# Optimization experiments

Hardware: AMD Instinct MI355X
Metric: run time of the kernel (lower is better)

Reference implementation:

```python
import jax, jax.numpy as jnp
import numpy as np

HEADS = 16
HEAD_SIZE = 64
INF = 1e12  # bert4keras K.infinity() uses a large finite value


def _rotate_interleaved(x):
    # result[..., 2i] = -x[..., 2i+1]; result[..., 2i+1] = x[..., 2i]
    x2 = jnp.stack([-x[..., 1::2], x[..., ::2]], axis=-1)
    return x2.reshape(x.shape)


def setup_inputs() -> dict:
    key = jax.random.key(0)
    k1, k2 = jax.random.split(key)
    B, N, D = 8, 1024, 1024
    x = jax.random.normal(k1, (B, N, D), dtype=jnp.float32)
    W = jax.random.normal(k2, (D, 2 * HEADS * HEAD_SIZE), dtype=jnp.float32) * (1.0 / np.sqrt(D))
    b = jnp.zeros((2 * HEADS * HEAD_SIZE,), dtype=jnp.float32)
    seq_mask = jnp.ones((B, N), dtype=jnp.float32)
    return {"x": x, "W": W, "b": b, "seq_mask": seq_mask}


def reference(x, W, b, seq_mask):
    B, N, _ = x.shape
    H, d = HEADS, HEAD_SIZE
    proj = x @ W + b                       # [B, N, 2*H*d]
    z = proj.reshape(B, N, H, 2 * d)       # split into heads then stack
    qw, kw = z[..., :d], z[..., d:]        # [B, N, H, d]

    # RoPE (interleaved sin/cos)
    pos = jnp.arange(N, dtype=jnp.float32)
    freqs = jnp.power(10000.0, -2.0 * jnp.arange(d // 2, dtype=jnp.float32) / d)
    ang = pos[:, None] * freqs[None, :]    # [N, d/2]
    cos_pos = jnp.repeat(jnp.cos(ang), 2, axis=-1)[None, :, None, :]  # [1,N,1,d]
    sin_pos = jnp.repeat(jnp.sin(ang), 2, axis=-1)[None, :, None, :]
    qw = qw * cos_pos + _rotate_interleaved(qw) * sin_pos
    kw = kw * cos_pos + _rotate_interleaved(kw) * sin_pos

    logits = jnp.einsum('bmhd,bnhd->bhmn', qw, kw)   # [B, H, N, N]

    # sequence masking on query (axis 2) and key (axis 3)
    logits = logits - (1.0 - seq_mask[:, None, :, None]) * INF
    logits = logits - (1.0 - seq_mask[:, None, None, :]) * INF

    # triangular mask: keep upper triangle including diagonal
    tri = jnp.triu(jnp.ones((N, N), dtype=logits.dtype))
    logits = logits - (1.0 - tri) * INF
    return logits / jnp.sqrt(jnp.float32(d))
```

## Files before the change

kernel.cpp:

```cpp
#include <hip/hip_runtime.h>

typedef __bf16 bf16;
typedef __bf16 bf16x4 __attribute__((ext_vector_type(4)));
typedef __bf16 bf16x8 __attribute__((ext_vector_type(8)));
typedef float f32x4 __attribute__((ext_vector_type(4)));

#define GL(p) ((const __attribute__((address_space(1))) void*)(p))
#define LD(p) ((__attribute__((address_space(3))) void*)(p))

static __device__ __forceinline__ void nt_store4(float* p, f32x4 v) {
    __builtin_nontemporal_store(v, (f32x4*)p);
}

__global__ __launch_bounds__(256) void k_prep(
    const float4* __restrict__ x4, bf16x4* __restrict__ o4,
    const float* __restrict__ W, bf16* __restrict__ Wt,
    float* __restrict__ cost, float* __restrict__ sint)
{
    __shared__ bf16 tile[64][65];
    const int bid = (int)blockIdx.x;
    const int t = threadIdx.x;
    if (bid < 2048) {
        for (int i = bid * 256 + t; i < 2097152; i += 2048 * 256) {
            float4 v = x4[i];
            bf16x4 o;
            o[0] = (bf16)v.x; o[1] = (bf16)v.y; o[2] = (bf16)v.z; o[3] = (bf16)v.w;
            o4[i] = o;
        }
    } else if (bid < 2560) {
        const int wid = bid - 2048;
        const int k0 = (wid & 15) * 64;
        const int n0 = (wid >> 4) * 64;
        const int c = t & 63, r4 = t >> 6;
#pragma unroll
        for (int p = 0; p < 16; ++p) {
            int r = p * 4 + r4;
            tile[r][c] = (bf16)W[(size_t)(k0 + r) * 2048 + n0 + c];
        }
        __syncthreads();
#pragma unroll
        for (int p = 0; p < 16; ++p) {
            int n = p * 4 + r4;
            Wt[(size_t)(n0 + n) * 1024 + k0 + c] = tile[c][n];
        }
    } else {
        int idx = (bid - 2560) * 256 + t;
        int pos = idx >> 5, i = idx & 31;
        float freq = powf(10000.f, -(float)i / 32.f);
        float ang = (float)pos * freq;
        cost[idx] = cosf(ang);
        sint[idx] = sinf(ang);
    }
}

__global__ __launch_bounds__(512) void k_gemm1(
    const bf16* __restrict__ Xb, const bf16* __restrict__ Wt,
    const float* __restrict__ bias,
    const float* __restrict__ cost, const float* __restrict__ sint,
    bf16* __restrict__ Qb, bf16* __restrict__ Kb,
    const float* __restrict__ smask, float* __restrict__ out)
{
    __shared__ bf16 lA[2][256 * 64];
    __shared__ bf16 lB[2][128 * 64];
    const int t = threadIdx.x;
    const int lane = t & 63;
    const int wave = t >> 6;
    const int wr = (wave >> 1) * 64;
    const int wc = (wave & 1) * 64;
    const int bm = (int)blockIdx.x * 256;
    const int bn = (int)blockIdx.y * 128;
    const int rl = lane & 15;
    const int hi = lane >> 4;
    const int flat7 = ((int)blockIdx.y * 32 + (int)blockIdx.x) * 7;
    const float NINF = 1.25e11f;

    f32x4 acc[4][4] = {};

#define STAGE1(kt, c) do {                                                              \
    _Pragma("unroll")                                                                   \
    for (int p = 0; p < 4; ++p) {                                                       \
        int e = t * 8 + p * 4096;                                                       \
        int row = e >> 6; int g = (e >> 3) & 7;                                         \
        __builtin_amdgcn_global_load_lds(                                               \
            GL(Xb + (size_t)(bm + row) * 1024 + (kt) * 64 + ((g ^ (row & 7)) << 3)),    \
            LD(&lA[c][e]), 16, 0, 0);                                                   \
    }                                                                                   \
    _Pragma("unroll")                                                                   \
    for (int p = 0; p < 2; ++p) {                                                       \
        int e = t * 8 + p * 4096;                                                       \
        int row = e >> 6; int g = (e >> 3) & 7;                                         \
        __builtin_amdgcn_global_load_lds(                                               \
            GL(Wt + (size_t)(bn + row) * 1024 + (kt) * 64 + ((g ^ (row & 7)) << 3)),    \
            LD(&lB[c][e]), 16, 0, 0);                                                   \
    }                                                                                   \
} while (0)

    STAGE1(0, 0);
    STAGE1(1, 1);
    asm volatile("s_waitcnt vmcnt(6)" ::: "memory");
    __builtin_amdgcn_sched_barrier(0);
    __builtin_amdgcn_s_barrier();
    asm volatile("" ::: "memory");

    for (int kt = 0; kt < 16; ++kt) {
        const int cur = kt & 1;

        if (kt < 14) {
            int inst = flat7 + (kt >> 1);
            int bh2 = inst & 127;
            int k28 = inst >> 7;
            int tm = 1;
            while (k28 >= ((tm * (tm + 1)) >> 1)) ++tm;
            int tn = k28 - ((tm * (tm - 1)) >> 1);
            int b2 = bh2 >> 4;
            int s0 = (kt & 1) * 4;
#pragma unroll
            for (int s = 0; s < 4; ++s) {
                int pos = (s0 + s) * 512 + t;
                int row = pos >> 5, c4 = (pos & 31) << 2;
                float smm = smask[b2 * 1024 + tm * 128 + row];
                f32x4 smn = *(const f32x4*)&smask[b2 * 1024 + tn * 128 + c4];
                f32x4 v;
#pragma unroll
                for (int r = 0; r < 4; ++r) v[r] = (smm + smn[r] - 3.f) * NINF;
                nt_store4(&out[((size_t)bh2 << 20) + ((size_t)(tm * 128 + row) << 10) + tn * 128 + c4], v);
            }
        }

        bf16x8 af[2][4], bfr[2][4];
#pragma unroll
        for (int ks = 0; ks < 2; ++ks) {
#pragma unroll
            for (int m = 0; m < 4; ++m) {
                int R = wr + m * 16 + rl;
                af[ks][m] = *(const bf16x8*)&lA[cur][(R << 6) + (((ks * 4 + hi) ^ (R & 7)) << 3)];
            }
#pragma unroll
            for (int n = 0; n < 4; ++n) {
                int S = wc + n * 16 + rl;
                bfr[ks][n] = *(const bf16x8*)&lB[cur][(S << 6) + (((ks * 4 + hi) ^ (S & 7)) << 3)];
            }
        }
#pragma unroll
        for (int ks = 0; ks < 2; ++ks)
#pragma unroll
            for (int m = 0; m < 4; ++m)
#pragma unroll
                for (int n = 0; n < 4; ++n)
                    acc[m][n] = __builtin_amdgcn_mfma_f32_16x16x32_bf16(af[ks][m], bfr[ks][n], acc[m][n], 0, 0, 0);

        if (kt < 15) {
            __builtin_amdgcn_s_barrier();
            if (kt + 2 < 16) {
                STAGE1(kt + 2, cur);
                asm volatile("s_waitcnt vmcnt(6)" ::: "memory");
            } else {
                asm volatile("s_waitcnt vmcnt(0)" ::: "memory");
            }
            __builtin_amdgcn_sched_barrier(0);
            __builtin_amdgcn_s_barrier();
            asm volatile("" ::: "memory");
        }
    }
#undef STAGE1

#pragma unroll
    for (int m = 0; m < 4; ++m) {
#pragma unroll
        for (int n = 0; n < 4; ++n) {
            int colg = bn + wc + n * 16 + rl;
            float bv = bias[colg];
            int h = colg >> 7;
            int rem = colg & 127;
            int qk = rem >> 6;
            int dcol = rem & 63;
            int fi = dcol >> 1;
            float sgn = (dcol & 1) ? 1.f : -1.f;
            bf16* dstb = qk ? Kb : Qb;
#pragma unroll
            for (int r = 0; r < 4; ++r) {
                int rowg = bm + wr + m * 16 + hi * 4 + r;
                int pos = rowg & 1023, bidx = rowg >> 10;
                float val = acc[m][n][r] + bv;
                float part = __shfl_xor(val, 1);
                float cv = cost[pos * 32 + fi], sv = sint[pos * 32 + fi];
                float outv = val * cv + sgn * part * sv;
                dstb[(((size_t)(bidx * 16 + h)) * 1024 + pos) * 64 + dcol] = (bf16)outv;
            }
        }
    }
}

__global__ __launch_bounds__(256) void k_gemm2(
    const bf16* __restrict__ Qb, const bf16* __restrict__ Kb,
    const float* __restrict__ smask, float* __restrict__ out)
{
    __shared__ __align__(16) char smem[33792];
    bf16* lQ = (bf16*)smem;
    bf16* lK = (bf16*)(smem + 16384);
    float* ldsF = (float*)smem;
    float* npen_l = (float*)(smem + 32768);
    float* mpen_l = (float*)(smem + 33280);

    const int t = threadIdx.x;
    const int lane = t & 63, wave = t >> 6;
    const int wm = (wave >> 1) * 64, wn = (wave & 1) * 64;
    const int bid = (int)blockIdx.x;
    const int xcd = bid & 7;
    const int idx0 = bid >> 3;
    const int bh = xcd * 16 + (idx0 & 15);
    int rem36 = idx0 >> 4;
    int tm = 0;
    while (rem36 >= 8 - tm) { rem36 -= 8 - tm; ++tm; }
    const int tn = tm + rem36;
    const int bm = tm * 128;
    const int bn = tn * 128;
    const int b = bh >> 4;
    const int rl = lane & 15, hi = lane >> 4;
    const float NINF = 1.25e11f;

    if (t < 128) npen_l[t] = 1.f - smask[b * 1024 + bn + t];
    else         mpen_l[t - 128] = 1.f - smask[b * 1024 + bm + (t - 128)];

    const size_t qoff = (size_t)bh * 1024 * 64;
#pragma unroll
    for (int p = 0; p < 4; ++p) {
        int e = t * 8 + p * 2048;
        int gr = e >> 3;
        int row = gr >> 3, c16 = gr & 7;
        int se = (row << 6) + ((c16 ^ (row & 7)) << 3);
        __builtin_amdgcn_global_load_lds(GL(Qb + qoff + (size_t)bm * 64 + se), LD(&lQ[e]), 16, 0, 0);
        __builtin_amdgcn_global_load_lds(GL(Kb + qoff + (size_t)bn * 64 + se), LD(&lK[e]), 16, 0, 0);
    }
    __syncthreads();

    f32x4 acc[4][4] = {};
#pragma unroll
    for (int ks = 0; ks < 2; ++ks) {
        bf16x8 af[4], bq[4];
#pragma unroll
        for (int i = 0; i < 4; ++i) {
            int R = wn + i * 16 + rl;
            af[i] = *(const bf16x8*)&lK[(R << 6) + ((((ks << 2) + hi) ^ (R & 7)) << 3)];
        }
#pragma unroll
        for (int j = 0; j < 4; ++j) {
            int Rq = wm + j * 16 + rl;
            bq[j] = *(const bf16x8*)&lQ[(Rq << 6) + ((((ks << 2) + hi) ^ (Rq & 7)) << 3)];
        }
#pragma unroll
        for (int i = 0; i < 4; ++i)
#pragma unroll
            for (int j = 0; j < 4; ++j)
                acc[i][j] = __builtin_amdgcn_mfma_f32_16x16x32_bf16(af[i], bq[j], acc[i][j], 0, 0, 0);
    }
    __syncthreads();

    for (int P = 0; P < 2; ++P) {
        if ((wave >> 1) == P) {
#pragma unroll
            for (int i = 0; i < 4; ++i)
#pragma unroll
                for (int j = 0; j < 4; ++j) {
                    int lrow = j * 16 + rl;
                    int lcol4 = wn * 4 + i * 64 + hi * 16;
                    char* p = (char*)ldsF + (lrow << 9) + (lcol4 ^ ((lrow & 7) << 4));
                    *(f32x4*)p = acc[i][j];
                }
        }
        __syncthreads();
#pragma unroll
        for (int k = 0; k < 8; ++k) {
            int idx = k * 256 + t;
            int lr = idx >> 5, slot = idx & 31;
            f32x4 v = ((const f32x4*)ldsF)[idx];
            int col = (((slot << 4) ^ ((lr & 7) << 4)) >> 2);
            int grow = bm + P * 64 + lr;
            int gcol = bn + col;
            float mp = mpen_l[P * 64 + lr];
            f32x4 np = *(const f32x4*)&npen_l[col];
            f32x4 vo;
#pragma unroll
            for (int r = 0; r < 4; ++r) {
                float pen = mp + np[r] + ((gcol + r < grow) ? 1.f : 0.f);
                vo[r] = v[r] * 0.125f - pen * NINF;
            }
            nt_store4(&out[((size_t)bh << 20) + ((size_t)grow << 10) + gcol], vo);
        }
        __syncthreads();
    }
}

extern "C" void kernel_launch(void* const* d_in, const int* in_sizes, int n_in,
                              void* d_out, int out_size, void* d_ws, size_t ws_size,
                              hipStream_t stream) {
    (void)in_sizes; (void)n_in; (void)out_size; (void)ws_size;
    const float* x    = (const float*)d_in[0];
    const float* W    = (const float*)d_in[1];
    const float* bias = (const float*)d_in[2];
    const float* sm   = (const float*)d_in[3];
    float* out = (float*)d_out;

    char* ws = (char*)d_ws;
    size_t o = 0;
    bf16* Xb = (bf16*)(ws + o); o += 8388608ull * 2;
    bf16* Wt = (bf16*)(ws + o); o += 2097152ull * 2;
    bf16* Qb = (bf16*)(ws + o); o += 8388608ull * 2;
    bf16* Kb = (bf16*)(ws + o); o += 8388608ull * 2;
    float* cost = (float*)(ws + o); o += 32768ull * 4;
    float* sint = (float*)(ws + o); o += 32768ull * 4;

    hipLaunchKernelGGL(k_prep, dim3(2688), dim3(256), 0, stream,
                       (const float4*)x, (bf16x4*)Xb, W, Wt, cost, sint);
    hipLaunchKernelGGL(k_gemm1, dim3(32, 16), dim3(512), 0, stream,
                       Xb, Wt, bias, cost, sint, Qb, Kb, sm, out);
    hipLaunchKernelGGL(k_gemm2, dim3(4608), dim3(256), 0, stream,
                       Qb, Kb, sm, out);
}
```

Baseline: 166.4 us.

## Store Q/K in MFMA fragment layout and move masked-tile fill to prep kernel

GEMM1 now writes rotated Q and K in a pre-swizzled fragment-major layout, so each lane in gemm2 loads its bf16x8 MFMA operand straight from global memory. This removes the LDS staging and one barrier in gemm2. The writes of the fully masked lower-triangle tiles move out of the gemm1 main loop into extra blocks of the prep kernel, which takes stores off the GEMM1 critical path. The cost is that gemm2 now reads operands from global/L2 without LDS reuse across waves, and the prep kernel becomes much larger (6272 blocks).

```diff
diff --git a/kernel.cpp b/kernel.cpp
--- a/kernel.cpp
+++ b/kernel.cpp
@@ -15,11 +15,13 @@
 __global__ __launch_bounds__(256) void k_prep(
     const float4* __restrict__ x4, bf16x4* __restrict__ o4,
     const float* __restrict__ W, bf16* __restrict__ Wt,
-    float* __restrict__ cost, float* __restrict__ sint)
+    float* __restrict__ cost, float* __restrict__ sint,
+    const float* __restrict__ smask, float* __restrict__ out)
 {
     __shared__ bf16 tile[64][65];
     const int bid = (int)blockIdx.x;
     const int t = threadIdx.x;
+    const float NINF = 1.25e11f;
     if (bid < 2048) {
         for (int i = bid * 256 + t; i < 2097152; i += 2048 * 256) {
             float4 v = x4[i];
@@ -43,13 +45,32 @@
             int n = p * 4 + r4;
             Wt[(size_t)(n0 + n) * 1024 + k0 + c] = tile[c][n];
         }
-    } else {
+    } else if (bid < 2688) {
         int idx = (bid - 2560) * 256 + t;
         int pos = idx >> 5, i = idx & 31;
         float freq = powf(10000.f, -(float)i / 32.f);
         float ang = (float)pos * freq;
         cost[idx] = cosf(ang);
         sint[idx] = sinf(ang);
+    } else {
+        int inst = bid - 2688;
+        int bh = inst & 127;
+        int k28 = inst >> 7;
+        int tm = 1;
+        while (k28 >= ((tm * (tm + 1)) >> 1)) ++tm;
+        int tn = k28 - ((tm * (tm - 1)) >> 1);
+        int b2 = bh >> 4;
+#pragma unroll
+        for (int it = 0; it < 16; ++it) {
+            int pos = it * 256 + t;
+            int row = pos >> 5, c4 = (pos & 31) << 2;
+            float smm = smask[b2 * 1024 + tm * 128 + row];
+            f32x4 smn = *(const f32x4*)&smask[b2 * 1024 + tn * 128 + c4];
+            f32x4 v;
+#pragma unroll
+            for (int r = 0; r < 4; ++r) v[r] = (smm + smn[r] - 3.f) * NINF;
+            nt_store4(&out[((size_t)bh << 20) + ((size_t)(tm * 128 + row) << 10) + tn * 128 + c4], v);
+        }
     }
 }
 
@@ -57,8 +78,7 @@
     const bf16* __restrict__ Xb, const bf16* __restrict__ Wt,
     const float* __restrict__ bias,
     const float* __restrict__ cost, const float* __restrict__ sint,
-    bf16* __restrict__ Qb, bf16* __restrict__ Kb,
-    const float* __restrict__ smask, float* __restrict__ out)
+    bf16* __restrict__ Qf, bf16* __restrict__ Kf)
 {
     __shared__ bf16 lA[2][256 * 64];
     __shared__ bf16 lB[2][128 * 64];
@@ -71,8 +91,6 @@
     const int bn = (int)blockIdx.y * 128;
     const int rl = lane & 15;
     const int hi = lane >> 4;
-    const int flat7 = ((int)blockIdx.y * 32 + (int)blockIdx.x) * 7;
-    const float NINF = 1.25e11f;
 
     f32x4 acc[4][4] = {};
 
@@ -104,29 +122,6 @@
 
     for (int kt = 0; kt < 16; ++kt) {
         const int cur = kt & 1;
-
-        if (kt < 14) {
-            int inst = flat7 + (kt >> 1);
-            int bh2 = inst & 127;
-            int k28 = inst >> 7;
-            int tm = 1;
-            while (k28 >= ((tm * (tm + 1)) >> 1)) ++tm;
-            int tn = k28 - ((tm * (tm - 1)) >> 1);
-            int b2 = bh2 >> 4;
-            int s0 = (kt & 1) * 4;
-#pragma unroll
-            for (int s = 0; s < 4; ++s) {
-                int pos = (s0 + s) * 512 + t;
-                int row = pos >> 5, c4 = (pos & 31) << 2;
-                float smm = smask[b2 * 1024 + tm * 128 + row];
-                f32x4 smn = *(const f32x4*)&smask[b2 * 1024 + tn * 128 + c4];
-                f32x4 v;
-#pragma unroll
-                for (int r = 0; r < 4; ++r) v[r] = (smm + smn[r] - 3.f) * NINF;
-                nt_store4(&out[((size_t)bh2 << 20) + ((size_t)(tm * 128 + row) << 10) + tn * 128 + c4], v);
-            }
-        }
-
         bf16x8 af[2][4], bfr[2][4];
 #pragma unroll
         for (int ks = 0; ks < 2; ++ks) {
@@ -176,7 +171,10 @@
             int dcol = rem & 63;
             int fi = dcol >> 1;
             float sgn = (dcol & 1) ? 1.f : -1.f;
-            bf16* dstb = qk ? Kb : Qb;
+            bf16* dstb = qk ? Kf : Qf;
+            int ks = dcol >> 5;
+            int kg2 = (dcol >> 3) & 3;
+            int elem = dcol & 7;
 #pragma unroll
             for (int r = 0; r < 4; ++r) {
                 int rowg = bm + wr + m * 16 + hi * 4 + r;
@@ -185,19 +183,19 @@
                 float part = __shfl_xor(val, 1);
                 float cv = cost[pos * 32 + fi], sv = sint[pos * 32 + fi];
                 float outv = val * cv + sgn * part * sv;
-                dstb[(((size_t)(bidx * 16 + h)) * 1024 + pos) * 64 + dcol] = (bf16)outv;
+                size_t base = ((size_t)(bidx * 16 + h)) << 16;
+                dstb[base + (size_t)((pos >> 4) * 1024 + ks * 512
+                                     + (hi * 4 + r + 16 * kg2) * 8 + elem)] = (bf16)outv;
             }
         }
     }
 }
 
 __global__ __launch_bounds__(256) void k_gemm2(
-    const bf16* __restrict__ Qb, const bf16* __restrict__ Kb,
+    const bf16* __restrict__ Qf, const bf16* __restrict__ Kf,
     const float* __restrict__ smask, float* __restrict__ out)
 {
     __shared__ __align__(16) char smem[33792];
-    bf16* lQ = (bf16*)smem;
-    bf16* lK = (bf16*)(smem + 16384);
     float* ldsF = (float*)smem;
     float* npen_l = (float*)(smem + 32768);
     float* mpen_l = (float*)(smem + 33280);
@@ -222,41 +220,30 @@
     if (t < 128) npen_l[t] = 1.f - smask[b * 1024 + bn + t];
     else         mpen_l[t - 128] = 1.f - smask[b * 1024 + bm + (t - 128)];
 
-    const size_t qoff = (size_t)bh * 1024 * 64;
-#pragma unroll
-    for (int p = 0; p < 4; ++p) {
-        int e = t * 8 + p * 2048;
-        int gr = e >> 3;
-        int row = gr >> 3, c16 = gr & 7;
-        int se = (row << 6) + ((c16 ^ (row & 7)) << 3);
-        __builtin_amdgcn_global_load_lds(GL(Qb + qoff + (size_t)bm * 64 + se), LD(&lQ[e]), 16, 0, 0);
-        __builtin_amdgcn_global_load_lds(GL(Kb + qoff + (size_t)bn * 64 + se), LD(&lK[e]), 16, 0, 0);
-    }
-    __syncthreads();
+    const bf16* Qb_bh = Qf + ((size_t)bh << 16);
+    const bf16* Kb_bh = Kf + ((size_t)bh << 16);
+    const int pK = (bn + wn) >> 4;
+    const int pQ = (bm + wm) >> 4;
 
     f32x4 acc[4][4] = {};
 #pragma unroll
     for (int ks = 0; ks < 2; ++ks) {
         bf16x8 af[4], bq[4];
 #pragma unroll
-        for (int i = 0; i < 4; ++i) {
-            int R = wn + i * 16 + rl;
-            af[i] = *(const bf16x8*)&lK[(R << 6) + ((((ks << 2) + hi) ^ (R & 7)) << 3)];
-        }
-#pragma unroll
-        for (int j = 0; j < 4; ++j) {
-            int Rq = wm + j * 16 + rl;
-            bq[j] = *(const bf16x8*)&lQ[(Rq << 6) + ((((ks << 2) + hi) ^ (Rq & 7)) << 3)];
-        }
+        for (int i = 0; i < 4; ++i)
+            af[i] = *(const bf16x8*)&Kb_bh[(pK + i) * 1024 + ks * 512 + lane * 8];
+#pragma unroll
+        for (int j = 0; j < 4; ++j)
+            bq[j] = *(const bf16x8*)&Qb_bh[(pQ + j) * 1024 + ks * 512 + lane * 8];
 #pragma unroll
         for (int i = 0; i < 4; ++i)
 #pragma unroll
             for (int j = 0; j < 4; ++j)
                 acc[i][j] = __builtin_amdgcn_mfma_f32_16x16x32_bf16(af[i], bq[j], acc[i][j], 0, 0, 0);
     }
-    __syncthreads();
 
     for (int P = 0; P < 2; ++P) {
+        if (P) __syncthreads();
         if ((wave >> 1) == P) {
 #pragma unroll
             for (int i = 0; i < 4; ++i)
@@ -287,7 +274,6 @@
             }
             nt_store4(&out[((size_t)bh << 20) + ((size_t)grow << 10) + gcol], vo);
         }
-        __syncthreads();
     }
 }
 
@@ -305,15 +291,15 @@
     size_t o = 0;
     bf16* Xb = (bf16*)(ws + o); o += 8388608ull * 2;
     bf16* Wt = (bf16*)(ws + o); o += 2097152ull * 2;
-    bf16* Qb = (bf16*)(ws + o); o += 8388608ull * 2;
-    bf16* Kb = (bf16*)(ws + o); o += 8388608ull * 2;
+    bf16* Qf = (bf16*)(ws + o); o += 8388608ull * 2;
+    bf16* Kf = (bf16*)(ws + o); o += 8388608ull * 2;
     float* cost = (float*)(ws + o); o += 32768ull * 4;
     float* sint = (float*)(ws + o); o += 32768ull * 4;
 
-    hipLaunchKernelGGL(k_prep, dim3(2688), dim3(256), 0, stream,
-                       (const float4*)x, (bf16x4*)Xb, W, Wt, cost, sint);
+    hipLaunchKernelGGL(k_prep, dim3(6272), dim3(256), 0, stream,
+                       (const float4*)x, (bf16x4*)Xb, W, Wt, cost, sint, sm, out);
     hipLaunchKernelGGL(k_gemm1, dim3(32, 16), dim3(512), 0, stream,
-                       Xb, Wt, bias, cost, sint, Qb, Kb, sm, out);
+                       Xb, Wt, bias, cost, sint, Qf, Kf);
     hipLaunchKernelGGL(k_gemm2, dim3(4608), dim3(256), 0, stream,
-                       Qb, Kb, sm, out);
-}
+                       Qf, Kf, sm, out);
+}
```

New measurement: 189.8 us. 14.1% more time.
